# Performance work log

Measured on AMD Instinct MI355X. Metric: run time of the kernel, lower is better.

Reference implementation:

```python
import jax, jax.numpy as jnp
import numpy as np

N_GAUSS = 1024
IMG = 192
TANFOV = 0.5  # tan(FoV/2), both axes
ZNEAR, ZFAR = 0.01, 100.0

C0 = 0.28209479177387814
C1 = 0.4886025119029199
C2 = (1.0925484305920792, -1.0925484305920792, 0.31539156525252005, -1.0925484305920792, 0.5462742152960396)
C3 = (-0.5900435899266435, 2.890611442640554, -0.4570457994644658, 0.3731763325901154, -0.4570457994644658, 1.445305721320277, -0.5900435899266435)


def _eval_sh3(sh, d):
    # sh: [N,16,3] coeffs, d: [N,3] unit dirs -> clamped rgb [N,3]
    x, y, z = d[:, 0:1], d[:, 1:2], d[:, 2:3]
    xx, yy, zz = x * x, y * y, z * z
    xy, yz, xz = x * y, y * z, x * z
    res = (C0 * sh[:, 0]
           - C1 * y * sh[:, 1] + C1 * z * sh[:, 2] - C1 * x * sh[:, 3]
           + C2[0] * xy * sh[:, 4] + C2[1] * yz * sh[:, 5]
           + C2[2] * (2.0 * zz - xx - yy) * sh[:, 6]
           + C2[3] * xz * sh[:, 7] + C2[4] * (xx - yy) * sh[:, 8]
           + C3[0] * y * (3.0 * xx - yy) * sh[:, 9]
           + C3[1] * xy * z * sh[:, 10]
           + C3[2] * y * (4.0 * zz - xx - yy) * sh[:, 11]
           + C3[3] * z * (2.0 * zz - 3.0 * xx - 3.0 * yy) * sh[:, 12]
           + C3[4] * x * (4.0 * zz - xx - yy) * sh[:, 13]
           + C3[5] * z * (xx - yy) * sh[:, 14]
           + C3[6] * x * (xx - yy - 3.0 * zz) * sh[:, 15])
    return jnp.maximum(res + 0.5, 0.0)


def _quat_to_rot(q):
    r, x, y, z = q[:, 0], q[:, 1], q[:, 2], q[:, 3]
    return jnp.stack([
        1 - 2 * (y * y + z * z), 2 * (x * y - r * z), 2 * (x * z + r * y),
        2 * (x * y + r * z), 1 - 2 * (x * x + z * z), 2 * (y * z - r * x),
        2 * (x * z - r * y), 2 * (y * z + r * x), 1 - 2 * (x * x + y * y),
    ], axis=-1).reshape(-1, 3, 3)


def setup_inputs() -> dict:
    key = jax.random.key(0)
    ks = jax.random.split(key, 6)
    xy = jax.random.uniform(ks[0], (N_GAUSS, 2), minval=-2.0, maxval=2.0)
    z = jax.random.uniform(ks[1], (N_GAUSS, 1), minval=2.0, maxval=10.0)
    means3D = jnp.concatenate([xy, z], axis=1)
    scales = jax.random.uniform(ks[2], (N_GAUSS, 3), minval=0.01, maxval=0.08)
    q = jax.random.normal(ks[3], (N_GAUSS, 4))
    rotations = q / jnp.linalg.norm(q, axis=1, keepdims=True)
    opacities = jax.random.uniform(ks[4], (N_GAUSS, 1), minval=0.1, maxval=0.99)
    shs = jax.random.normal(ks[5], (N_GAUSS, 16, 3)) * 0.3
    viewmatrix = jnp.eye(4, dtype=jnp.float32)
    proj = np.zeros((4, 4), np.float32)
    proj[0, 0] = 1.0 / TANFOV
    proj[1, 1] = 1.0 / TANFOV
    proj[2, 2] = ZFAR / (ZFAR - ZNEAR)
    proj[2, 3] = -ZFAR * ZNEAR / (ZFAR - ZNEAR)
    proj[3, 2] = 1.0
    return dict(means3D=means3D, scales=scales, rotations=rotations,
                opacities=opacities, shs=shs, viewmatrix=viewmatrix,
                projmatrix=jnp.asarray(proj), campos=jnp.zeros(3, jnp.float32),
                bg_color=jnp.zeros(3, jnp.float32),
                image_height=IMG, image_width=IMG)


def reference(means3D, scales, rotations, opacities, shs, viewmatrix,
              projmatrix, campos, bg_color, image_height, image_width):
    H, W = int(image_height), int(image_width)
    fx = W / (2.0 * TANFOV)
    fy = H / (2.0 * TANFOV)
    N = means3D.shape[0]

    # SH -> RGB (convert_SHs_python branch, active_sh_degree = 3)
    dir_pp = means3D - campos[None, :]
    dir_pp = dir_pp / jnp.linalg.norm(dir_pp, axis=1, keepdims=True)
    colors = _eval_sh3(shs, dir_pp)  # [N,3]

    # 3D covariance Sigma = (R S)(R S)^T  (scale_modifier = 1.0)
    R = _quat_to_rot(rotations)
    M = R * scales[:, None, :]
    cov3d = jnp.einsum('nij,nkj->nik', M, M)  # [N,3,3]

    # projection of means
    hom = jnp.concatenate([means3D, jnp.ones((N, 1), means3D.dtype)], axis=1)
    p_view = hom @ viewmatrix.T
    depth = p_view[:, 2]
    p_hom = hom @ projmatrix.T
    p_proj = p_hom[:, :3] / (p_hom[:, 3:4] + 1e-7)
    gx = ((p_proj[:, 0] + 1.0) * W - 1.0) * 0.5  # ndc2Pix
    gy = ((p_proj[:, 1] + 1.0) * H - 1.0) * 0.5
    means2D = jnp.stack([gx, gy], axis=1)

    in_front = depth > 0.2
    tz = jnp.where(in_front, depth, 1.0)
    lim = 1.3 * TANFOV
    tx = jnp.clip(p_view[:, 0] / tz, -lim, lim) * tz
    ty = jnp.clip(p_view[:, 1] / tz, -lim, lim) * tz

    # EWA splatting: J (top 2 rows) composed with view rotation
    zeros = jnp.zeros_like(tz)
    J = jnp.stack([
        jnp.stack([fx / tz, zeros, -fx * tx / (tz * tz)], axis=-1),
        jnp.stack([zeros, fy / tz, -fy * ty / (tz * tz)], axis=-1),
    ], axis=1)  # [N,2,3]
    T = jnp.einsum('nij,jk->nik', J, viewmatrix[:3, :3])
    cov2d = jnp.einsum('nij,njk,nlk->nil', T, cov3d, T)  # [N,2,2]
    a = cov2d[:, 0, 0] + 0.3  # low-pass filter on diagonal
    b = cov2d[:, 0, 1]
    c = cov2d[:, 1, 1] + 0.3

    det = a * c - b * b
    pos_det = det > 0
    inv_det = jnp.where(pos_det, 1.0 / jnp.where(pos_det, det, 1.0), 0.0)
    conA, conB, conC = c * inv_det, -b * inv_det, a * inv_det

    mid = 0.5 * (a + c)
    lam = mid + jnp.sqrt(jnp.maximum(mid * mid - det, 0.1))
    visible = in_front & pos_det
    radii = jnp.where(visible, jnp.ceil(3.0 * jnp.sqrt(lam)), 0.0)
    visibility_filter = radii > 0

    # per-pixel depth-sorted alpha compositing (dense stand-in for tiles)
    yy, xx = jnp.meshgrid(jnp.arange(H, dtype=means3D.dtype),
                          jnp.arange(W, dtype=means3D.dtype), indexing='ij')
    px = xx.reshape(-1)
    py = yy.reshape(-1)
    dx = gx[None, :] - px[:, None]  # [P,N]
    dy = gy[None, :] - py[:, None]
    power = (-0.5 * (conA[None, :] * dx * dx + conC[None, :] * dy * dy)
             - conB[None, :] * dx * dy)
    keep = ((jnp.abs(dx) <= radii[None, :]) & (jnp.abs(dy) <= radii[None, :])
            & visible[None, :] & (power <= 0.0))
    alpha = jnp.minimum(0.99, opacities[:, 0][None, :] * jnp.exp(jnp.minimum(power, 0.0)))
    alpha = jnp.where(keep & (alpha >= 1.0 / 255.0), alpha, 0.0)

    order = jnp.argsort(jnp.where(visible, depth, jnp.inf))
    a_s = alpha[:, order]
    Tcum = jnp.cumprod(1.0 - a_s, axis=1)
    T_before = jnp.concatenate(
        [jnp.ones((a_s.shape[0], 1), a_s.dtype), Tcum[:, :-1]], axis=1)
    wgt = a_s * T_before
    img = wgt @ colors[order] + Tcum[:, -1:] * bg_color[None, :]
    rendered = img.reshape(H, W, 3).transpose(2, 0, 1)  # CHW like torch
    return rendered, radii.astype(jnp.int32), visibility_filter, means2D
```

## Files before the change

### kernel.cpp

```cpp
#include <hip/hip_runtime.h>

#define NG      1024
#define W_IMG   192
#define H_IMG   192
#define HW      (W_IMG * H_IMG)
#define PSTR    12
#define NSEG    8
#define TILES_X (W_IMG / 8)
#define TILES_Y (H_IMG / 8)
#define NTILES  (TILES_X * TILES_Y)


__global__ __launch_bounds__(256) void preprocess_kernel(
    const float* __restrict__ means3D, const float* __restrict__ scales,
    const float* __restrict__ rotations, const float* __restrict__ opacities,
    const float* __restrict__ shs, const float* __restrict__ viewm,
    const float* __restrict__ projm, const float* __restrict__ campos,
    float* __restrict__ params, float* __restrict__ outp)
{
    const int i = blockIdx.x * 256 + threadIdx.x;
    if (i >= NG) return;

    const float mx = means3D[i * 3 + 0];
    const float my = means3D[i * 3 + 1];
    const float mz = means3D[i * 3 + 2];

    float dxc = mx - campos[0], dyc = my - campos[1], dzc = mz - campos[2];
    float nrm = sqrtf(dxc * dxc + dyc * dyc + dzc * dzc);
    float x = dxc / nrm, y = dyc / nrm, z = dzc / nrm;
    float xx = x * x, yy = y * y, zz = z * z;
    float xy = x * y, yz = y * z, xz = x * z;

    float basis[16];
    basis[0]  = 0.28209479177387814f;
    basis[1]  = -0.4886025119029199f * y;
    basis[2]  =  0.4886025119029199f * z;
    basis[3]  = -0.4886025119029199f * x;
    basis[4]  =  1.0925484305920792f * xy;
    basis[5]  = -1.0925484305920792f * yz;
    basis[6]  =  0.31539156525252005f * (2.f * zz - xx - yy);
    basis[7]  = -1.0925484305920792f * xz;
    basis[8]  =  0.5462742152960396f * (xx - yy);
    basis[9]  = -0.5900435899266435f * y * (3.f * xx - yy);
    basis[10] =  2.890611442640554f  * xy * z;
    basis[11] = -0.4570457994644658f * y * (4.f * zz - xx - yy);
    basis[12] =  0.3731763325901154f * z * (2.f * zz - 3.f * xx - 3.f * yy);
    basis[13] = -0.4570457994644658f * x * (4.f * zz - xx - yy);
    basis[14] =  1.445305721320277f  * z * (xx - yy);
    basis[15] = -0.5900435899266435f * x * (xx - yy - 3.f * zz);

    float cr = 0.f, cg = 0.f, cb = 0.f;
#pragma unroll
    for (int k = 0; k < 16; ++k) {
        float b = basis[k];
        cr += b * shs[(i * 16 + k) * 3 + 0];
        cg += b * shs[(i * 16 + k) * 3 + 1];
        cb += b * shs[(i * 16 + k) * 3 + 2];
    }
    cr = fmaxf(cr + 0.5f, 0.f);
    cg = fmaxf(cg + 0.5f, 0.f);
    cb = fmaxf(cb + 0.5f, 0.f);

    float qr = rotations[i * 4 + 0], qx = rotations[i * 4 + 1];
    float qy = rotations[i * 4 + 2], qz = rotations[i * 4 + 3];
    float sx = scales[i * 3 + 0], sy = scales[i * 3 + 1], sz = scales[i * 3 + 2];
    float R00 = 1.f - 2.f * (qy * qy + qz * qz), R01 = 2.f * (qx * qy - qr * qz), R02 = 2.f * (qx * qz + qr * qy);
    float R10 = 2.f * (qx * qy + qr * qz), R11 = 1.f - 2.f * (qx * qx + qz * qz), R12 = 2.f * (qy * qz - qr * qx);
    float R20 = 2.f * (qx * qz - qr * qy), R21 = 2.f * (qy * qz + qr * qx), R22 = 1.f - 2.f * (qx * qx + qy * qy);
    float M00 = R00 * sx, M01 = R01 * sy, M02 = R02 * sz;
    float M10 = R10 * sx, M11 = R11 * sy, M12 = R12 * sz;
    float M20 = R20 * sx, M21 = R21 * sy, M22 = R22 * sz;
    float S00 = M00 * M00 + M01 * M01 + M02 * M02;
    float S01 = M00 * M10 + M01 * M11 + M02 * M12;
    float S02 = M00 * M20 + M01 * M21 + M02 * M22;
    float S11 = M10 * M10 + M11 * M11 + M12 * M12;
    float S12 = M10 * M20 + M11 * M21 + M12 * M22;
    float S22 = M20 * M20 + M21 * M21 + M22 * M22;

    float pv0 = viewm[0] * mx + viewm[1] * my + viewm[2]  * mz + viewm[3];
    float pv1 = viewm[4] * mx + viewm[5] * my + viewm[6]  * mz + viewm[7];
    float pv2 = viewm[8] * mx + viewm[9] * my + viewm[10] * mz + viewm[11];
    float ph0 = projm[0]  * mx + projm[1]  * my + projm[2]  * mz + projm[3];
    float ph1 = projm[4]  * mx + projm[5]  * my + projm[6]  * mz + projm[7];
    float ph3 = projm[12] * mx + projm[13] * my + projm[14] * mz + projm[15];
    float pp0 = ph0 / (ph3 + 1e-7f);
    float pp1 = ph1 / (ph3 + 1e-7f);
    float gx = ((pp0 + 1.f) * (float)W_IMG - 1.f) * 0.5f;
    float gy = ((pp1 + 1.f) * (float)H_IMG - 1.f) * 0.5f;

    float depth = pv2;
    bool in_front = depth > 0.2f;
    float tz = in_front ? depth : 1.f;
    const float lim = 1.3f * 0.5f;
    float txv = fminf(fmaxf(pv0 / tz, -lim), lim) * tz;
    float tyv = fminf(fmaxf(pv1 / tz, -lim), lim) * tz;
    const float fx = (float)W_IMG / (2.f * 0.5f);
    const float fy = (float)H_IMG / (2.f * 0.5f);
    float J00 = fx / tz, J02 = -fx * txv / (tz * tz);
    float J11 = fy / tz, J12 = -fy * tyv / (tz * tz);

    float T00 = J00 * viewm[0] + J02 * viewm[8];
    float T01 = J00 * viewm[1] + J02 * viewm[9];
    float T02 = J00 * viewm[2] + J02 * viewm[10];
    float T10 = J11 * viewm[4] + J12 * viewm[8];
    float T11 = J11 * viewm[5] + J12 * viewm[9];
    float T12 = J11 * viewm[6] + J12 * viewm[10];

    float u0 = T00 * S00 + T01 * S01 + T02 * S02;
    float u1 = T00 * S01 + T01 * S11 + T02 * S12;
    float u2 = T00 * S02 + T01 * S12 + T02 * S22;
    float v0 = T10 * S00 + T11 * S01 + T12 * S02;
    float v1 = T10 * S01 + T11 * S11 + T12 * S12;
    float v2 = T10 * S02 + T11 * S12 + T12 * S22;
    float c00 = u0 * T00 + u1 * T01 + u2 * T02;
    float c01 = u0 * T10 + u1 * T11 + u2 * T12;
    float c11 = v0 * T10 + v1 * T11 + v2 * T12;

    float a = c00 + 0.3f;
    float b = c01;
    float c = c11 + 0.3f;
    float det = a * c - b * b;
    bool pos_det = det > 0.f;
    float inv_det = pos_det ? 1.f / det : 0.f;
    float conA = c * inv_det, conB = -b * inv_det, conC = a * inv_det;
    float mid = 0.5f * (a + c);
    float lam = mid + sqrtf(fmaxf(mid * mid - det, 0.1f));
    bool visible = in_front && pos_det;
    float radii = visible ? ceilf(3.f * sqrtf(lam)) : 0.f;

    float opa = opacities[i];

    outp[3 * HW + i] = radii;
    outp[3 * HW + NG + i] = (radii > 0.f) ? 1.f : 0.f;
    outp[3 * HW + 2 * NG + i * 2 + 0] = gx;
    outp[3 * HW + 2 * NG + i * 2 + 1] = gy;

    float* p = params + i * PSTR;
    p[0] = gx;   p[1] = gy;   p[2]  = radii; p[3]  = visible ? opa : 0.f;
    p[4] = conA; p[5] = conB; p[6]  = conC;  p[7]  = visible ? depth : 1e30f;
    p[8] = cr;   p[9] = cg;   p[10] = cb;    p[11] = 0.f;
}

__global__ __launch_bounds__(512) void raster_kernel(
    const float* __restrict__ params, const float* __restrict__ bg,
    float* __restrict__ outp)
{
    __shared__ float4 sp[NG * 3];
    __shared__ float  sdep[NG];
    __shared__ int    sidx[NG];
    __shared__ int    ssorted[NG];
    __shared__ float4 segacc[NSEG * 64];
    __shared__ int    s_cnt;

    const int t = threadIdx.x;
    if (t == 0) s_cnt = 0;
    {
        const float4* src = (const float4*)params;
        for (int k = t; k < NG * 3; k += 512) sp[k] = src[k];
    }
    __syncthreads();

    const int wave = t >> 6;
    const int lane = t & 63;
    const int tileX = blockIdx.x % TILES_X;
    const int tileY = blockIdx.x / TILES_X;
    const float tx0 = (float)(tileX * 8);
    const float ty0 = (float)(tileY * 8);

#pragma unroll
    for (int h = 0; h < 2; ++h) {
        const int gi = wave * 128 + h * 64 + lane;
        float4 g0 = sp[gi * 3];
        bool hit = (g0.w > 0.f) &&
                   (g0.x >= tx0 - g0.z) && (g0.x <= tx0 + 7.f + g0.z) &&
                   (g0.y >= ty0 - g0.z) && (g0.y <= ty0 + 7.f + g0.z);
        unsigned long long mask = __ballot(hit);
        int base = 0;
        if (lane == 0 && mask) base = atomicAdd(&s_cnt, __popcll(mask));
        base = __shfl(base, 0);
        if (hit) {
            int pos = base + __popcll(mask & ((1ULL << lane) - 1ULL));
            sidx[pos] = gi;
            sdep[pos] = sp[gi * 3 + 1].w;
        }
    }
    __syncthreads();

    const int M = s_cnt;

    for (int s = t; s < M; s += 512) {
        const float ds = sdep[s];
        const int   is = sidx[s];
        int rank = 0;
        for (int j = 0; j < M; ++j) {
            float dj = sdep[j];
            int   ij = sidx[j];
            rank += (dj < ds || (dj == ds && ij < is)) ? 1 : 0;
        }
        ssorted[rank] = is;
    }
    __syncthreads();

    const int lx = lane & 7, ly = lane >> 3;
    const int pxi = tileX * 8 + lx;
    const int pyi = tileY * 8 + ly;
    const float px = (float)pxi, py = (float)pyi;

    const int chunk = (M + NSEG - 1) / NSEG;
    const int kbeg = wave * chunk;
    const int kend = min(M, kbeg + chunk);

    float T = 1.f, accR = 0.f, accG = 0.f, accB = 0.f;
    for (int k = kbeg; k < kend; ++k) {
        const int gi = ssorted[k];
        float4 g0 = sp[gi * 3 + 0];
        float4 g1 = sp[gi * 3 + 1];
        float4 g2 = sp[gi * 3 + 2];
        float dx = g0.x - px, dy = g0.y - py;
        bool cover = (fabsf(dx) <= g0.z) && (fabsf(dy) <= g0.z);
        float power = -0.5f * (g1.x * dx * dx + g1.z * dy * dy) - g1.y * dx * dy;
        float alpha = fminf(0.99f, g0.w * __expf(fminf(power, 0.f)));
        bool keep = cover && (power <= 0.f) && (alpha >= (1.f / 255.f));
        alpha = keep ? alpha : 0.f;
        float w = alpha * T;
        accR += w * g2.x;
        accG += w * g2.y;
        accB += w * g2.z;
        T *= (1.f - alpha);
    }

    segacc[wave * 64 + lane] = make_float4(accR, accG, accB, T);
    __syncthreads();

    if (t < 64) {
        float Tc = 1.f, r = 0.f, g = 0.f, b = 0.f;
#pragma unroll
        for (int s = 0; s < NSEG; ++s) {
            float4 cc = segacc[s * 64 + t];
            r += Tc * cc.x;
            g += Tc * cc.y;
            b += Tc * cc.z;
            Tc *= cc.w;
        }
        const int pix = pyi * W_IMG + pxi;
        outp[pix]          = r + Tc * bg[0];
        outp[HW + pix]     = g + Tc * bg[1];
        outp[2 * HW + pix] = b + Tc * bg[2];
    }
}

extern "C" void kernel_launch(void* const* d_in, const int* in_sizes, int n_in,
                              void* d_out, int out_size, void* d_ws, size_t ws_size,
                              hipStream_t stream)
{
    const float* means3D   = (const float*)d_in[0];
    const float* scales    = (const float*)d_in[1];
    const float* rotations = (const float*)d_in[2];
    const float* opacities = (const float*)d_in[3];
    const float* shs       = (const float*)d_in[4];
    const float* viewm     = (const float*)d_in[5];
    const float* projm     = (const float*)d_in[6];
    const float* campos    = (const float*)d_in[7];
    const float* bg        = (const float*)d_in[8];

    float* outp   = (float*)d_out;
    float* params = (float*)d_ws;

    preprocess_kernel<<<NG / 256, 256, 0, stream>>>(
        means3D, scales, rotations, opacities, shs, viewm, projm, campos,
        params, outp);

    raster_kernel<<<NTILES, 512, 0, stream>>>(params, bg, outp);
}
```

Measured before the change: 84.70 us.

## Fuse preprocessing into raster kernel with one tile per wave

Merges the preprocess and raster kernels into one launch where every block recomputes all gaussian parameters directly into shared memory, removing the global params round trip and second launch. Each wave now owns one 8x8 tile, binning with ballot-prefix counts and sorting by a packed depth/index 64-bit key, then compositing serially without segment merging. This trades redundant per-block preprocessing and longer serial per-wave loops, plus fewer blocks than CUs, for lower launch and sync overhead.

```diff
diff --git a/kernel.cpp b/kernel.cpp
--- a/kernel.cpp
+++ b/kernel.cpp
@@ -4,200 +4,202 @@
 #define W_IMG   192
 #define H_IMG   192
 #define HW      (W_IMG * H_IMG)
-#define PSTR    12
-#define NSEG    8
-#define TILES_X (W_IMG / 8)
-#define TILES_Y (H_IMG / 8)
+#define TILES_X 24
+#define TILES_Y 24
 #define NTILES  (TILES_X * TILES_Y)
-
-
-__global__ __launch_bounds__(256) void preprocess_kernel(
+#define TPB     256
+#define TPBK    4
+#define NBLK    (NTILES / TPBK)
+
+__global__ __launch_bounds__(TPB, 1) void render_fused(
     const float* __restrict__ means3D, const float* __restrict__ scales,
     const float* __restrict__ rotations, const float* __restrict__ opacities,
     const float* __restrict__ shs, const float* __restrict__ viewm,
     const float* __restrict__ projm, const float* __restrict__ campos,
-    float* __restrict__ params, float* __restrict__ outp)
+    const float* __restrict__ bg, float* __restrict__ outp)
 {
-    const int i = blockIdx.x * 256 + threadIdx.x;
-    if (i >= NG) return;
-
-    const float mx = means3D[i * 3 + 0];
-    const float my = means3D[i * 3 + 1];
-    const float mz = means3D[i * 3 + 2];
-
-    float dxc = mx - campos[0], dyc = my - campos[1], dzc = mz - campos[2];
-    float nrm = sqrtf(dxc * dxc + dyc * dyc + dzc * dzc);
-    float x = dxc / nrm, y = dyc / nrm, z = dzc / nrm;
-    float xx = x * x, yy = y * y, zz = z * z;
-    float xy = x * y, yz = y * z, xz = x * z;
-
-    float basis[16];
-    basis[0]  = 0.28209479177387814f;
-    basis[1]  = -0.4886025119029199f * y;
-    basis[2]  =  0.4886025119029199f * z;
-    basis[3]  = -0.4886025119029199f * x;
-    basis[4]  =  1.0925484305920792f * xy;
-    basis[5]  = -1.0925484305920792f * yz;
-    basis[6]  =  0.31539156525252005f * (2.f * zz - xx - yy);
-    basis[7]  = -1.0925484305920792f * xz;
-    basis[8]  =  0.5462742152960396f * (xx - yy);
-    basis[9]  = -0.5900435899266435f * y * (3.f * xx - yy);
-    basis[10] =  2.890611442640554f  * xy * z;
-    basis[11] = -0.4570457994644658f * y * (4.f * zz - xx - yy);
-    basis[12] =  0.3731763325901154f * z * (2.f * zz - 3.f * xx - 3.f * yy);
-    basis[13] = -0.4570457994644658f * x * (4.f * zz - xx - yy);
-    basis[14] =  1.445305721320277f  * z * (xx - yy);
-    basis[15] = -0.5900435899266435f * x * (xx - yy - 3.f * zz);
-
-    float cr = 0.f, cg = 0.f, cb = 0.f;
+    __shared__ float4 sg0[NG];
+    __shared__ float4 sg1[NG];
+    __shared__ float4 sg2[NG];
+    __shared__ unsigned long long skey[TPBK][NG];
+    __shared__ unsigned short     ssrt[TPBK][NG];
+
+    const int t = threadIdx.x;
+
+    const float V0 = viewm[0],  V1 = viewm[1],  V2  = viewm[2],  V3  = viewm[3];
+    const float V4 = viewm[4],  V5 = viewm[5],  V6  = viewm[6],  V7  = viewm[7];
+    const float V8 = viewm[8],  V9 = viewm[9],  V10 = viewm[10], V11 = viewm[11];
+    const float P0 = projm[0],  P1 = projm[1],  P2  = projm[2],  P3  = projm[3];
+    const float P4 = projm[4],  P5 = projm[5],  P6  = projm[6],  P7  = projm[7];
+    const float P12 = projm[12], P13 = projm[13], P14 = projm[14], P15 = projm[15];
+    const float CX = campos[0], CY = campos[1], CZ = campos[2];
+
 #pragma unroll
-    for (int k = 0; k < 16; ++k) {
-        float b = basis[k];
-        cr += b * shs[(i * 16 + k) * 3 + 0];
-        cg += b * shs[(i * 16 + k) * 3 + 1];
-        cb += b * shs[(i * 16 + k) * 3 + 2];
-    }
-    cr = fmaxf(cr + 0.5f, 0.f);
-    cg = fmaxf(cg + 0.5f, 0.f);
-    cb = fmaxf(cb + 0.5f, 0.f);
-
-    float qr = rotations[i * 4 + 0], qx = rotations[i * 4 + 1];
-    float qy = rotations[i * 4 + 2], qz = rotations[i * 4 + 3];
-    float sx = scales[i * 3 + 0], sy = scales[i * 3 + 1], sz = scales[i * 3 + 2];
-    float R00 = 1.f - 2.f * (qy * qy + qz * qz), R01 = 2.f * (qx * qy - qr * qz), R02 = 2.f * (qx * qz + qr * qy);
-    float R10 = 2.f * (qx * qy + qr * qz), R11 = 1.f - 2.f * (qx * qx + qz * qz), R12 = 2.f * (qy * qz - qr * qx);
-    float R20 = 2.f * (qx * qz - qr * qy), R21 = 2.f * (qy * qz + qr * qx), R22 = 1.f - 2.f * (qx * qx + qy * qy);
-    float M00 = R00 * sx, M01 = R01 * sy, M02 = R02 * sz;
-    float M10 = R10 * sx, M11 = R11 * sy, M12 = R12 * sz;
-    float M20 = R20 * sx, M21 = R21 * sy, M22 = R22 * sz;
-    float S00 = M00 * M00 + M01 * M01 + M02 * M02;
-    float S01 = M00 * M10 + M01 * M11 + M02 * M12;
-    float S02 = M00 * M20 + M01 * M21 + M02 * M22;
-    float S11 = M10 * M10 + M11 * M11 + M12 * M12;
-    float S12 = M10 * M20 + M11 * M21 + M12 * M22;
-    float S22 = M20 * M20 + M21 * M21 + M22 * M22;
-
-    float pv0 = viewm[0] * mx + viewm[1] * my + viewm[2]  * mz + viewm[3];
-    float pv1 = viewm[4] * mx + viewm[5] * my + viewm[6]  * mz + viewm[7];
-    float pv2 = viewm[8] * mx + viewm[9] * my + viewm[10] * mz + viewm[11];
-    float ph0 = projm[0]  * mx + projm[1]  * my + projm[2]  * mz + projm[3];
-    float ph1 = projm[4]  * mx + projm[5]  * my + projm[6]  * mz + projm[7];
-    float ph3 = projm[12] * mx + projm[13] * my + projm[14] * mz + projm[15];
-    float pp0 = ph0 / (ph3 + 1e-7f);
-    float pp1 = ph1 / (ph3 + 1e-7f);
-    float gx = ((pp0 + 1.f) * (float)W_IMG - 1.f) * 0.5f;
-    float gy = ((pp1 + 1.f) * (float)H_IMG - 1.f) * 0.5f;
-
-    float depth = pv2;
-    bool in_front = depth > 0.2f;
-    float tz = in_front ? depth : 1.f;
-    const float lim = 1.3f * 0.5f;
-    float txv = fminf(fmaxf(pv0 / tz, -lim), lim) * tz;
-    float tyv = fminf(fmaxf(pv1 / tz, -lim), lim) * tz;
-    const float fx = (float)W_IMG / (2.f * 0.5f);
-    const float fy = (float)H_IMG / (2.f * 0.5f);
-    float J00 = fx / tz, J02 = -fx * txv / (tz * tz);
-    float J11 = fy / tz, J12 = -fy * tyv / (tz * tz);
-
-    float T00 = J00 * viewm[0] + J02 * viewm[8];
-    float T01 = J00 * viewm[1] + J02 * viewm[9];
-    float T02 = J00 * viewm[2] + J02 * viewm[10];
-    float T10 = J11 * viewm[4] + J12 * viewm[8];
-    float T11 = J11 * viewm[5] + J12 * viewm[9];
-    float T12 = J11 * viewm[6] + J12 * viewm[10];
-
-    float u0 = T00 * S00 + T01 * S01 + T02 * S02;
-    float u1 = T00 * S01 + T01 * S11 + T02 * S12;
-    float u2 = T00 * S02 + T01 * S12 + T02 * S22;
-    float v0 = T10 * S00 + T11 * S01 + T12 * S02;
-    float v1 = T10 * S01 + T11 * S11 + T12 * S12;
-    float v2 = T10 * S02 + T11 * S12 + T12 * S22;
-    float c00 = u0 * T00 + u1 * T01 + u2 * T02;
-    float c01 = u0 * T10 + u1 * T11 + u2 * T12;
-    float c11 = v0 * T10 + v1 * T11 + v2 * T12;
-
-    float a = c00 + 0.3f;
-    float b = c01;
-    float c = c11 + 0.3f;
-    float det = a * c - b * b;
-    bool pos_det = det > 0.f;
-    float inv_det = pos_det ? 1.f / det : 0.f;
-    float conA = c * inv_det, conB = -b * inv_det, conC = a * inv_det;
-    float mid = 0.5f * (a + c);
-    float lam = mid + sqrtf(fmaxf(mid * mid - det, 0.1f));
-    bool visible = in_front && pos_det;
-    float radii = visible ? ceilf(3.f * sqrtf(lam)) : 0.f;
-
-    float opa = opacities[i];
-
-    outp[3 * HW + i] = radii;
-    outp[3 * HW + NG + i] = (radii > 0.f) ? 1.f : 0.f;
-    outp[3 * HW + 2 * NG + i * 2 + 0] = gx;
-    outp[3 * HW + 2 * NG + i * 2 + 1] = gy;
-
-    float* p = params + i * PSTR;
-    p[0] = gx;   p[1] = gy;   p[2]  = radii; p[3]  = visible ? opa : 0.f;
-    p[4] = conA; p[5] = conB; p[6]  = conC;  p[7]  = visible ? depth : 1e30f;
-    p[8] = cr;   p[9] = cg;   p[10] = cb;    p[11] = 0.f;
-}
-
-__global__ __launch_bounds__(512) void raster_kernel(
-    const float* __restrict__ params, const float* __restrict__ bg,
-    float* __restrict__ outp)
-{
-    __shared__ float4 sp[NG * 3];
-    __shared__ float  sdep[NG];
-    __shared__ int    sidx[NG];
-    __shared__ int    ssorted[NG];
-    __shared__ float4 segacc[NSEG * 64];
-    __shared__ int    s_cnt;
-
-    const int t = threadIdx.x;
-    if (t == 0) s_cnt = 0;
-    {
-        const float4* src = (const float4*)params;
-        for (int k = t; k < NG * 3; k += 512) sp[k] = src[k];
+    for (int j = 0; j < NG / TPB; ++j) {
+        const int i = t + j * TPB;
+
+        const float mx = means3D[i * 3 + 0];
+        const float my = means3D[i * 3 + 1];
+        const float mz = means3D[i * 3 + 2];
+
+        float dxc = mx - CX, dyc = my - CY, dzc = mz - CZ;
+        float nrm = sqrtf(dxc * dxc + dyc * dyc + dzc * dzc);
+        float x = dxc / nrm, y = dyc / nrm, z = dzc / nrm;
+        float xx = x * x, yy = y * y, zz = z * z;
+        float xy = x * y, yz = y * z, xz = x * z;
+
+        float basis[16];
+        basis[0]  = 0.28209479177387814f;
+        basis[1]  = -0.4886025119029199f * y;
+        basis[2]  =  0.4886025119029199f * z;
+        basis[3]  = -0.4886025119029199f * x;
+        basis[4]  =  1.0925484305920792f * xy;
+        basis[5]  = -1.0925484305920792f * yz;
+        basis[6]  =  0.31539156525252005f * (2.f * zz - xx - yy);
+        basis[7]  = -1.0925484305920792f * xz;
+        basis[8]  =  0.5462742152960396f * (xx - yy);
+        basis[9]  = -0.5900435899266435f * y * (3.f * xx - yy);
+        basis[10] =  2.890611442640554f  * xy * z;
+        basis[11] = -0.4570457994644658f * y * (4.f * zz - xx - yy);
+        basis[12] =  0.3731763325901154f * z * (2.f * zz - 3.f * xx - 3.f * yy);
+        basis[13] = -0.4570457994644658f * x * (4.f * zz - xx - yy);
+        basis[14] =  1.445305721320277f  * z * (xx - yy);
+        basis[15] = -0.5900435899266435f * x * (xx - yy - 3.f * zz);
+
+        float sh[48];
+        const float4* shv = (const float4*)shs + i * 12;
+#pragma unroll
+        for (int w = 0; w < 12; ++w) {
+            float4 q4 = shv[w];
+            sh[4 * w + 0] = q4.x; sh[4 * w + 1] = q4.y;
+            sh[4 * w + 2] = q4.z; sh[4 * w + 3] = q4.w;
+        }
+        float cr = 0.f, cg = 0.f, cb = 0.f;
+#pragma unroll
+        for (int k = 0; k < 16; ++k) {
+            float b = basis[k];
+            cr += b * sh[3 * k + 0];
+            cg += b * sh[3 * k + 1];
+            cb += b * sh[3 * k + 2];
+        }
+        cr = fmaxf(cr + 0.5f, 0.f);
+        cg = fmaxf(cg + 0.5f, 0.f);
+        cb = fmaxf(cb + 0.5f, 0.f);
+
+        const float4 q = ((const float4*)rotations)[i];
+        float qr = q.x, qx = q.y, qy = q.z, qz = q.w;
+        float sx = scales[i * 3 + 0], sy = scales[i * 3 + 1], sz = scales[i * 3 + 2];
+        float R00 = 1.f - 2.f * (qy * qy + qz * qz), R01 = 2.f * (qx * qy - qr * qz), R02 = 2.f * (qx * qz + qr * qy);
+        float R10 = 2.f * (qx * qy + qr * qz), R11 = 1.f - 2.f * (qx * qx + qz * qz), R12 = 2.f * (qy * qz - qr * qx);
+        float R20 = 2.f * (qx * qz - qr * qy), R21 = 2.f * (qy * qz + qr * qx), R22 = 1.f - 2.f * (qx * qx + qy * qy);
+        float M00 = R00 * sx, M01 = R01 * sy, M02 = R02 * sz;
+        float M10 = R10 * sx, M11 = R11 * sy, M12 = R12 * sz;
+        float M20 = R20 * sx, M21 = R21 * sy, M22 = R22 * sz;
+        float S00 = M00 * M00 + M01 * M01 + M02 * M02;
+        float S01 = M00 * M10 + M01 * M11 + M02 * M12;
+        float S02 = M00 * M20 + M01 * M21 + M02 * M22;
+        float S11 = M10 * M10 + M11 * M11 + M12 * M12;
+        float S12 = M10 * M20 + M11 * M21 + M12 * M22;
+        float S22 = M20 * M20 + M21 * M21 + M22 * M22;
+
+        float pv0 = V0 * mx + V1 * my + V2  * mz + V3;
+        float pv1 = V4 * mx + V5 * my + V6  * mz + V7;
+        float pv2 = V8 * mx + V9 * my + V10 * mz + V11;
+        float ph0 = P0  * mx + P1  * my + P2  * mz + P3;
+        float ph1 = P4  * mx + P5  * my + P6  * mz + P7;
+        float ph3 = P12 * mx + P13 * my + P14 * mz + P15;
+        float pp0 = ph0 / (ph3 + 1e-7f);
+        float pp1 = ph1 / (ph3 + 1e-7f);
+        float gx = ((pp0 + 1.f) * (float)W_IMG - 1.f) * 0.5f;
+        float gy = ((pp1 + 1.f) * (float)H_IMG - 1.f) * 0.5f;
+
+        float depth = pv2;
+        bool in_front = depth > 0.2f;
+        float tz = in_front ? depth : 1.f;
+        const float lim = 1.3f * 0.5f;
+        float txv = fminf(fmaxf(pv0 / tz, -lim), lim) * tz;
+        float tyv = fminf(fmaxf(pv1 / tz, -lim), lim) * tz;
+        const float fx = (float)W_IMG / (2.f * 0.5f);
+        const float fy = (float)H_IMG / (2.f * 0.5f);
+        float J00 = fx / tz, J02 = -fx * txv / (tz * tz);
+        float J11 = fy / tz, J12 = -fy * tyv / (tz * tz);
+
+        float T00 = J00 * V0 + J02 * V8;
+        float T01 = J00 * V1 + J02 * V9;
+        float T02 = J00 * V2 + J02 * V10;
+        float T10 = J11 * V4 + J12 * V8;
+        float T11 = J11 * V5 + J12 * V9;
+        float T12 = J11 * V6 + J12 * V10;
+
+        float u0 = T00 * S00 + T01 * S01 + T02 * S02;
+        float u1 = T00 * S01 + T01 * S11 + T02 * S12;
+        float u2 = T00 * S02 + T01 * S12 + T02 * S22;
+        float w0 = T10 * S00 + T11 * S01 + T12 * S02;
+        float w1 = T10 * S01 + T11 * S11 + T12 * S12;
+        float w2 = T10 * S02 + T11 * S12 + T12 * S22;
+        float c00 = u0 * T00 + u1 * T01 + u2 * T02;
+        float c01 = u0 * T10 + u1 * T11 + u2 * T12;
+        float c11 = w0 * T10 + w1 * T11 + w2 * T12;
+
+        float a = c00 + 0.3f;
+        float b = c01;
+        float c = c11 + 0.3f;
+        float det = a * c - b * b;
+        bool pos_det = det > 0.f;
+        float inv_det = pos_det ? 1.f / det : 0.f;
+        float conA = c * inv_det, conB = -b * inv_det, conC = a * inv_det;
+        float mid = 0.5f * (a + c);
+        float lam = mid + sqrtf(fmaxf(mid * mid - det, 0.1f));
+        bool visible = in_front && pos_det;
+        float radii = visible ? ceilf(3.f * sqrtf(lam)) : 0.f;
+
+        float opa = opacities[i];
+
+        sg0[i] = make_float4(gx, gy, radii, visible ? opa : 0.f);
+        sg1[i] = make_float4(conA, conB, conC, depth);
+        sg2[i] = make_float4(cr, cg, cb, 0.f);
+
+        if (blockIdx.x == 0) {
+            outp[3 * HW + i]              = radii;
+            outp[3 * HW + NG + i]         = (radii > 0.f) ? 1.f : 0.f;
+            outp[3 * HW + 2 * NG + 2 * i]     = gx;
+            outp[3 * HW + 2 * NG + 2 * i + 1] = gy;
+        }
     }
     __syncthreads();
 
     const int wave = t >> 6;
     const int lane = t & 63;
-    const int tileX = blockIdx.x % TILES_X;
-    const int tileY = blockIdx.x / TILES_X;
+    const int tile = blockIdx.x * TPBK + wave;
+    const int tileX = tile % TILES_X;
+    const int tileY = tile / TILES_X;
     const float tx0 = (float)(tileX * 8);
     const float ty0 = (float)(tileY * 8);
 
-#pragma unroll
-    for (int h = 0; h < 2; ++h) {
-        const int gi = wave * 128 + h * 64 + lane;
-        float4 g0 = sp[gi * 3];
+    int m = 0;
+#pragma unroll 4
+    for (int it = 0; it < NG / 64; ++it) {
+        const int g = it * 64 + lane;
+        float4 g0 = sg0[g];
         bool hit = (g0.w > 0.f) &&
                    (g0.x >= tx0 - g0.z) && (g0.x <= tx0 + 7.f + g0.z) &&
                    (g0.y >= ty0 - g0.z) && (g0.y <= ty0 + 7.f + g0.z);
         unsigned long long mask = __ballot(hit);
-        int base = 0;
-        if (lane == 0 && mask) base = atomicAdd(&s_cnt, __popcll(mask));
-        base = __shfl(base, 0);
         if (hit) {
-            int pos = base + __popcll(mask & ((1ULL << lane) - 1ULL));
-            sidx[pos] = gi;
-            sdep[pos] = sp[gi * 3 + 1].w;
-        }
+            int pos = m + __popcll(mask & ((1ULL << lane) - 1ULL));
+            skey[wave][pos] =
+                ((unsigned long long)__float_as_uint(sg1[g].w) << 32) | (unsigned)g;
+        }
+        m += __popcll(mask);
     }
     __syncthreads();
 
-    const int M = s_cnt;
-
-    for (int s = t; s < M; s += 512) {
-        const float ds = sdep[s];
-        const int   is = sidx[s];
+    for (int s = lane; s < m; s += 64) {
+        const unsigned long long ks = skey[wave][s];
         int rank = 0;
-        for (int j = 0; j < M; ++j) {
-            float dj = sdep[j];
-            int   ij = sidx[j];
-            rank += (dj < ds || (dj == ds && ij < is)) ? 1 : 0;
-        }
-        ssorted[rank] = is;
+        for (int j2 = 0; j2 < m; ++j2)
+            rank += (skey[wave][j2] < ks) ? 1 : 0;
+        ssrt[wave][rank] = (unsigned short)(ks & 0xFFFFu);
     }
     __syncthreads();
 
@@ -206,16 +208,12 @@
     const int pyi = tileY * 8 + ly;
     const float px = (float)pxi, py = (float)pyi;
 
-    const int chunk = (M + NSEG - 1) / NSEG;
-    const int kbeg = wave * chunk;
-    const int kend = min(M, kbeg + chunk);
-
     float T = 1.f, accR = 0.f, accG = 0.f, accB = 0.f;
-    for (int k = kbeg; k < kend; ++k) {
-        const int gi = ssorted[k];
-        float4 g0 = sp[gi * 3 + 0];
-        float4 g1 = sp[gi * 3 + 1];
-        float4 g2 = sp[gi * 3 + 2];
+    for (int k = 0; k < m; ++k) {
+        const int gi = ssrt[wave][k];
+        float4 g0 = sg0[gi];
+        float4 g1 = sg1[gi];
+        float4 g2 = sg2[gi];
         float dx = g0.x - px, dy = g0.y - py;
         bool cover = (fabsf(dx) <= g0.z) && (fabsf(dy) <= g0.z);
         float power = -0.5f * (g1.x * dx * dx + g1.z * dy * dy) - g1.y * dx * dy;
@@ -229,24 +227,10 @@
         T *= (1.f - alpha);
     }
 
-    segacc[wave * 64 + lane] = make_float4(accR, accG, accB, T);
-    __syncthreads();
-
-    if (t < 64) {
-        float Tc = 1.f, r = 0.f, g = 0.f, b = 0.f;
-#pragma unroll
-        for (int s = 0; s < NSEG; ++s) {
-            float4 cc = segacc[s * 64 + t];
-            r += Tc * cc.x;
-            g += Tc * cc.y;
-            b += Tc * cc.z;
-            Tc *= cc.w;
-        }
-        const int pix = pyi * W_IMG + pxi;
-        outp[pix]          = r + Tc * bg[0];
-        outp[HW + pix]     = g + Tc * bg[1];
-        outp[2 * HW + pix] = b + Tc * bg[2];
-    }
+    const int pix = pyi * W_IMG + pxi;
+    outp[pix]          = accR + T * bg[0];
+    outp[HW + pix]     = accG + T * bg[1];
+    outp[2 * HW + pix] = accB + T * bg[2];
 }
 
 extern "C" void kernel_launch(void* const* d_in, const int* in_sizes, int n_in,
@@ -263,12 +247,9 @@
     const float* campos    = (const float*)d_in[7];
     const float* bg        = (const float*)d_in[8];
 
-    float* outp   = (float*)d_out;
-    float* params = (float*)d_ws;
-
-    preprocess_kernel<<<NG / 256, 256, 0, stream>>>(
+    float* outp = (float*)d_out;
+
+    render_fused<<<NBLK, TPB, 0, stream>>>(
         means3D, scales, rotations, opacities, shs, viewm, projm, campos,
-        params, outp);
-
-    raster_kernel<<<NTILES, 512, 0, stream>>>(params, bg, outp);
+        bg, outp);
 }
```

New measurement: 88.67 us. 1.05x slower.
